# Performance work log

Hardware: AMD Instinct MI355X
Metric: run time of the kernel (lower is better)

## Reference

```python
import jax, jax.numpy as jnp
import numpy as np

N_NODES = 100000
N_EDGES = 1600000
DIM_NODE = 128
DIM_HID = 128
N_CLASSES = 10


def gcn_conv(x, src, dst, W, b, num_nodes):
    # PyG GCNConv: h = W x; out[i] = sum_j norm_ij * h[j] + b, with self-loops
    # and symmetric normalization norm_ij = deg(i)^-1/2 * deg(j)^-1/2.
    ones = jnp.ones(src.shape[0], dtype=x.dtype)
    deg = jax.ops.segment_sum(ones, dst, num_segments=num_nodes)  # in-degree incl self-loop
    dinv = jnp.where(deg > 0, jax.lax.rsqrt(deg), 0.0)
    norm = dinv[src] * dinv[dst]                                  # [E+N]
    h = x @ W                                                     # [N, out]
    msg = h[src] * norm[:, None]                                  # gather + scale
    out = jax.ops.segment_sum(msg, dst, num_segments=num_nodes)   # scatter-add
    return out + b


def setup_inputs() -> dict:
    key = jax.random.key(0)
    ks = jax.random.split(key, 8)
    x = jax.random.normal(ks[0], (N_NODES, DIM_NODE), dtype=jnp.float32)
    edge_index = jax.random.randint(ks[1], (2, N_EDGES), 0, N_NODES, dtype=jnp.int32)
    def lin(k, fan_in, fan_out):
        s = 1.0 / np.sqrt(fan_in)
        return jax.random.uniform(k, (fan_in, fan_out), jnp.float32, -s, s)
    W1 = lin(ks[2], DIM_NODE, DIM_HID)
    W2 = lin(ks[3], DIM_HID, DIM_HID)
    W3 = lin(ks[4], DIM_HID, DIM_HID)
    fW1 = lin(ks[5], DIM_HID, DIM_HID)
    fW2 = lin(ks[6], DIM_HID, N_CLASSES)
    z = lambda n: jnp.zeros((n,), jnp.float32)
    return {"x": x, "edge_index": edge_index,
            "W1": W1, "b1": z(DIM_HID), "W2": W2, "b2": z(DIM_HID),
            "W3": W3, "b3": z(DIM_HID), "fW1": fW1, "fb1": z(DIM_HID),
            "fW2": fW2, "fb2": z(N_CLASSES)}


def reference(x, edge_index, W1, b1, W2, b2, W3, b3, fW1, fb1, fW2, fb2):
    num_nodes = x.shape[0]
    loop = jnp.arange(num_nodes, dtype=edge_index.dtype)
    src = jnp.concatenate([edge_index[0], loop])  # add self-loops once
    dst = jnp.concatenate([edge_index[1], loop])
    h = jax.nn.relu(gcn_conv(x, src, dst, W1, b1, num_nodes))
    h = jax.nn.relu(gcn_conv(h, src, dst, W2, b2, num_nodes))
    h = jax.nn.relu(gcn_conv(h, src, dst, W3, b3, num_nodes))
    # FFN head (Dropout is identity in eval mode)
    h = jax.nn.relu(h @ fW1 + fb1)
    out = h @ fW2 + fb2
    return out
```

## Files before the change

kernel.cpp:

```cpp
#include <hip/hip_runtime.h>
#include <hip/hip_bf16.h>
#include <hip/hip_fp16.h>

#define DIM 128
#define ROWS 16
#define NCAP 64
#define NSH  6

typedef __attribute__((ext_vector_type(8))) short bf16x8;
typedef __attribute__((ext_vector_type(4))) float f32x4;
typedef _Float16 half_t;

union Frag { unsigned int u[4]; bf16x8 v; uint4 q; };
union H8   { uint4 q; half_t h[8]; };

__device__ __forceinline__ void cvt_hilo(const float* __restrict__ x, Frag& hi, Frag& lo) {
#pragma unroll
    for (int p = 0; p < 4; ++p) {
        float x0 = x[2 * p], x1 = x[2 * p + 1];
        unsigned int h0 = (__float_as_uint(x0) + 0x8000u) & 0xffff0000u;
        unsigned int h1 = (__float_as_uint(x1) + 0x8000u) & 0xffff0000u;
        hi.u[p] = (h0 >> 16) | h1;
        float d0 = x0 - __uint_as_float(h0);
        float d1 = x1 - __uint_as_float(h1);
        lo.u[p] = (__float_as_uint(d0) >> 16) | (__float_as_uint(d1) & 0xffff0000u);
    }
}

__global__ __launch_bounds__(256) void init_kernel(
    const float* __restrict__ W0, const float* __restrict__ W1,
    const float* __restrict__ W2, const float* __restrict__ W3,
    uint4* __restrict__ WFhi, uint4* __restrict__ WFlo,
    int* __restrict__ ncur, int N) {
    int t = blockIdx.x * 256 + threadIdx.x;
    if (t < 8192) {
        int wi = t >> 11;
        const float* W = (wi == 0) ? W0 : (wi == 1) ? W1 : (wi == 2) ? W2 : W3;
        int tt   = t & 2047;
        int lane = tt & 63;
        int f    = tt >> 6;
        int kc   = f >> 3;
        int wc   = (f >> 2) & 1;
        int ct   = f & 3;
        int m    = lane & 15;
        int quad = lane >> 4;
        int col  = wc * 64 + ct * 16 + m;
        int k0   = kc * 32 + quad * 8;
        float wv8[8];
#pragma unroll
        for (int j = 0; j < 8; ++j) wv8[j] = W[(size_t)(k0 + j) * DIM + col];
        Frag hi, lo;
        cvt_hilo(wv8, hi, lo);
        WFhi[t] = hi.q;
        WFlo[t] = lo.q;
    }
    int n = t - 8192;
    if (n >= 0 && n < N) ncur[n] = n << NSH;
}

__global__ __launch_bounds__(256) void dinv_kernel(
    const int* __restrict__ ncur, float* __restrict__ dinv, int N) {
    int n = blockIdx.x * 256 + threadIdx.x;
    if (n < N) {
        int deg = min(ncur[n] - (n << NSH), NCAP);
        dinv[n] = rsqrtf((float)(deg + 1));
    }
}

__global__ __launch_bounds__(256, 8) void mega_kernel(
    const float* __restrict__ X,
    const uint4* __restrict__ WFhi, const uint4* __restrict__ WFlo,
    half_t* __restrict__ Y,
    const int* __restrict__ src, const int* __restrict__ dst,
    int* __restrict__ ncur, int* __restrict__ colidx,
    int E, int N, int nGemm)
{
    __shared__ uint4 Sbuf[512];
    const int bid = blockIdx.x;
    const int tid = threadIdx.x;

    if ((bid % 5) == 4) {
        const int sIdx  = bid / 5;
        const int nScat = gridDim.x / 5;
        for (int e = sIdx * 256 + tid; e < E; e += nScat * 256) {
            int d = dst[e];
            int p = atomicAdd(&ncur[d], 1);
            if (p < (d << NSH) + NCAP) colidx[p] = src[e];
        }
        return;
    }
    const int g = bid - (bid + 1) / 5;
    if (g >= nGemm) return;
    const int row0 = g * ROWS;

    {
        const int row  = tid >> 4;
        const int oct  = tid & 15;
        const int node = row0 + row;
        float acc8[8];
        if (node < N) {
            const float* xp = X + (size_t)node * DIM + oct * 8;
            float4 a0 = *(const float4*)xp;
            float4 a1 = *(const float4*)(xp + 4);
            acc8[0] = a0.x; acc8[1] = a0.y; acc8[2] = a0.z; acc8[3] = a0.w;
            acc8[4] = a1.x; acc8[5] = a1.y; acc8[6] = a1.z; acc8[7] = a1.w;
        } else {
#pragma unroll
            for (int j = 0; j < 8; ++j) acc8[j] = 0.f;
        }
        Frag hi, lo;
        cvt_hilo(acc8, hi, lo);
        int fi = (oct >> 2) * 64 + (oct & 3) * 16 + (row ^ oct);
        Sbuf[fi]       = hi.q;
        Sbuf[256 + fi] = lo.q;
    }
    __syncthreads();

    const int lane = tid & 63;
    const int w    = tid >> 6;
    const int m    = lane & 15;
    const int quad = lane >> 4;
    f32x4 acc[2];
    acc[0] = f32x4{0.f, 0.f, 0.f, 0.f};
    acc[1] = f32x4{0.f, 0.f, 0.f, 0.f};
#pragma unroll
    for (int kc = 0; kc < 4; ++kc) {
        Frag ahi, alo;
        int fi = kc * 64 + quad * 16 + (m ^ (kc * 4 + quad));
        ahi.q = Sbuf[fi];
        alo.q = Sbuf[256 + fi];
#pragma unroll
        for (int j = 0; j < 2; ++j) {
            int ctg = w * 2 + j;
            Frag bhi, blo;
            int idx = (kc * 8 + ctg) * 64 + lane;
            bhi.q = WFhi[idx];
            blo.q = WFlo[idx];
            acc[j] = __builtin_amdgcn_mfma_f32_16x16x32_bf16(ahi.v, bhi.v, acc[j], 0, 0, 0);
            acc[j] = __builtin_amdgcn_mfma_f32_16x16x32_bf16(ahi.v, blo.v, acc[j], 0, 0, 0);
            acc[j] = __builtin_amdgcn_mfma_f32_16x16x32_bf16(alo.v, bhi.v, acc[j], 0, 0, 0);
        }
    }

#pragma unroll
    for (int r = 0; r < 4; ++r) {
        int grow = row0 + quad * 4 + r;
        if (grow >= N) continue;
#pragma unroll
        for (int j = 0; j < 2; ++j)
            Y[(size_t)grow * DIM + w * 32 + j * 16 + m] = (half_t)acc[j][r];
    }
}

template<bool SRCSCALE, bool FFN>
__global__ __launch_bounds__(256, 8) void fused16(
    const int* __restrict__ ncur, const int* __restrict__ colidx,
    const half_t* __restrict__ Hin, const float* __restrict__ bg,
    const float* __restrict__ dinv,
    const uint4* __restrict__ WFhi, const uint4* __restrict__ WFlo,
    const float* __restrict__ fb1,
    const float* __restrict__ fW2, const float* __restrict__ fb2,
    void* __restrict__ YV, int N)
{
    __shared__ uint4 Sbuf[512];
    __shared__ float Wl[FFN ? (DIM * 10 + 16) : 1];

    const int tid  = threadIdx.x;
    const int row0 = blockIdx.x * ROWS;

    if constexpr (FFN) {
        for (int i = tid; i < DIM * 10; i += 256) Wl[i] = fW2[i];
        if (tid < 10) Wl[DIM * 10 + tid] = fb2[tid];
    }

    {
        const int row  = tid >> 4;
        const int oct  = tid & 15;
        const int node = row0 + row;
        float acc8[8];
        if (node < N) {
            const half_t* hb = Hin + oct * 8;
            H8 sv; sv.q = *(const uint4*)(hb + (size_t)node * DIM);
            const float dvd = dinv[node];
            float a[8];
#pragma unroll
            for (int j = 0; j < 8; ++j)
                a[j] = SRCSCALE ? dvd * (float)sv.h[j] : (float)sv.h[j];
            const int beg = node << NSH;
            const int deg = min(ncur[node] - beg, NCAP);
            int e = 0;
            for (; e + 4 <= deg; e += 4) {
                int4 c = *(const int4*)&colidx[beg + e];
                H8 v0, v1, v2, v3;
                v0.q = *(const uint4*)(hb + (size_t)c.x * DIM);
                v1.q = *(const uint4*)(hb + (size_t)c.y * DIM);
                v2.q = *(const uint4*)(hb + (size_t)c.z * DIM);
                v3.q = *(const uint4*)(hb + (size_t)c.w * DIM);
                if constexpr (SRCSCALE) {
                    float d0 = dinv[c.x], d1 = dinv[c.y], d2 = dinv[c.z], d3 = dinv[c.w];
#pragma unroll
                    for (int j = 0; j < 8; ++j)
                        a[j] = fmaf(d3, (float)v3.h[j],
                               fmaf(d2, (float)v2.h[j],
                               fmaf(d1, (float)v1.h[j],
                               fmaf(d0, (float)v0.h[j], a[j]))));
                } else {
#pragma unroll
                    for (int j = 0; j < 8; ++j)
                        a[j] += ((float)v0.h[j] + (float)v1.h[j]) + ((float)v2.h[j] + (float)v3.h[j]);
                }
            }
            for (; e < deg; ++e) {
                int c = colidx[beg + e];
                H8 v0; v0.q = *(const uint4*)(hb + (size_t)c * DIM);
                if constexpr (SRCSCALE) {
                    float d0 = dinv[c];
#pragma unroll
                    for (int j = 0; j < 8; ++j) a[j] = fmaf(d0, (float)v0.h[j], a[j]);
                } else {
#pragma unroll
                    for (int j = 0; j < 8; ++j) a[j] += (float)v0.h[j];
                }
            }
            const float* bp = bg + oct * 8;
#pragma unroll
            for (int j = 0; j < 8; ++j)
                acc8[j] = fmaxf(fmaf(a[j], dvd, bp[j]), 0.f);
        } else {
#pragma unroll
            for (int j = 0; j < 8; ++j) acc8[j] = 0.f;
        }
        Frag hi, lo;
        cvt_hilo(acc8, hi, lo);
        int fi = (oct >> 2) * 64 + (oct & 3) * 16 + (row ^ oct);
        Sbuf[fi]       = hi.q;
        Sbuf[256 + fi] = lo.q;
    }
    __syncthreads();

    const int lane = tid & 63;
    const int w    = tid >> 6;
    const int m    = lane & 15;
    const int quad = lane >> 4;

    f32x4 acc[2];
    acc[0] = f32x4{0.f, 0.f, 0.f, 0.f};
    acc[1] = f32x4{0.f, 0.f, 0.f, 0.f};

#pragma unroll
    for (int kc = 0; kc < 4; ++kc) {
        Frag ahi, alo;
        int fi = kc * 64 + quad * 16 + (m ^ (kc * 4 + quad));
        ahi.q = Sbuf[fi];
        alo.q = Sbuf[256 + fi];
#pragma unroll
        for (int j = 0; j < 2; ++j) {
            int ctg = w * 2 + j;
            Frag bhi, blo;
            int idx = (kc * 8 + ctg) * 64 + lane;
            bhi.q = WFhi[idx];
            blo.q = WFlo[idx];
            acc[j] = __builtin_amdgcn_mfma_f32_16x16x32_bf16(ahi.v, bhi.v, acc[j], 0, 0, 0);
            acc[j] = __builtin_amdgcn_mfma_f32_16x16x32_bf16(ahi.v, blo.v, acc[j], 0, 0, 0);
            acc[j] = __builtin_amdgcn_mfma_f32_16x16x32_bf16(alo.v, bhi.v, acc[j], 0, 0, 0);
        }
    }

    if constexpr (!FFN) {
        half_t* Y = (half_t*)YV;
#pragma unroll
        for (int r = 0; r < 4; ++r) {
            int grow = row0 + quad * 4 + r;
            if (grow >= N) continue;
            float s = dinv[grow];
#pragma unroll
            for (int j = 0; j < 2; ++j)
                Y[(size_t)grow * DIM + w * 32 + j * 16 + m] = (half_t)(acc[j][r] * s);
        }
    } else {
        float* Y = (float*)YV;
        __syncthreads();
        float* hbuf = (float*)Sbuf;
#pragma unroll
        for (int r = 0; r < 4; ++r) {
            int lrow = quad * 4 + r;
#pragma unroll
            for (int j = 0; j < 2; ++j) {
                int col = w * 32 + j * 16 + m;
                hbuf[lrow * DIM + col] = fmaxf(acc[j][r] + fb1[col], 0.f);
            }
        }
        __syncthreads();
        if (tid < ROWS * 10) {
            int r  = tid / 10;
            int cc = tid - r * 10;
            int grow = row0 + r;
            if (grow < N) {
                float a = 0.f;
#pragma unroll 8
                for (int kk = 0; kk < DIM; ++kk) {
                    int k = (kk + r * 4) & 127;
                    a = fmaf(hbuf[r * DIM + k], Wl[k * 10 + cc], a);
                }
                Y[(size_t)grow * 10 + cc] = a + Wl[DIM * 10 + cc];
            }
        }
    }
}

extern "C" void kernel_launch(void* const* d_in, const int* in_sizes, int n_in,
                              void* d_out, int out_size, void* d_ws, size_t ws_size,
                              hipStream_t stream) {
    const float* x   = (const float*)d_in[0];
    const int*   ei  = (const int*)  d_in[1];
    const float* W1  = (const float*)d_in[2];
    const float* b1  = (const float*)d_in[3];
    const float* W2  = (const float*)d_in[4];
    const float* b2  = (const float*)d_in[5];
    const float* W3  = (const float*)d_in[6];
    const float* b3  = (const float*)d_in[7];
    const float* fW1 = (const float*)d_in[8];
    const float* fb1 = (const float*)d_in[9];
    const float* fW2 = (const float*)d_in[10];
    const float* fb2 = (const float*)d_in[11];
    float* out = (float*)d_out;

    const int N = in_sizes[0] / DIM;
    const int E = in_sizes[1] / 2;
    const int* srcI = ei;
    const int* dstI = ei + E;

    char* ws = (char*)d_ws;
    size_t off = 0;
    auto carve = [&](size_t bytes) { void* p = ws + off; off = (off + bytes + 255) & ~(size_t)255; return p; };
    int*   ncur       = (int*)  carve((size_t)N * 4);
    float* dinv       = (float*)carve((size_t)N * 4);
    int*   colidx     = (int*)  carve((size_t)N * NCAP * 4);
    uint4* wfhi       = (uint4*)carve((size_t)4 * 2048 * 16);
    uint4* wflo       = (uint4*)carve((size_t)4 * 2048 * 16);
    half_t* bufA      = (half_t*)carve((size_t)N * DIM * 2);
    half_t* bufB      = (half_t*)carve((size_t)N * DIM * 2);

    dim3 blk(256);
    int nGemm = (N + ROWS - 1) / ROWS;
    int gInit = (8192 + N + 255) / 256;
    int gN    = (N + 255) / 256;
    int gMega = (nGemm * 5 + 3) / 4;

    init_kernel<<<gInit, blk, 0, stream>>>(W1, W2, W3, fW1, wfhi, wflo, ncur, N);

    mega_kernel<<<gMega, blk, 0, stream>>>(x, wfhi + 0 * 2048, wflo + 0 * 2048, bufA,
                                           srcI, dstI, ncur, colidx, E, N, nGemm);

    dinv_kernel<<<gN, blk, 0, stream>>>(ncur, dinv, N);

    fused16<true, false><<<nGemm, blk, 0, stream>>>(ncur, colidx, bufA, b1, dinv,
                                                    wfhi + 1 * 2048, wflo + 1 * 2048,
                                                    nullptr, nullptr, nullptr, bufB, N);

    fused16<false, false><<<nGemm, blk, 0, stream>>>(ncur, colidx, bufB, b2, dinv,
                                                     wfhi + 2 * 2048, wflo + 2 * 2048,
                                                     nullptr, nullptr, nullptr, bufA, N);

    fused16<false, true><<<nGemm, blk, 0, stream>>>(ncur, colidx, bufA, b3, dinv,
                                                    wfhi + 3 * 2048, wflo + 3 * 2048,
                                                    fb1, fW2, fb2, out, N);
}
```

Before: 425.9 us.

## Partition edge scatter by destination slice per XCD with shared-memory staging ring

The scatter blocks now each own one of eight destination-node slices, picked from the block index, which appears meant to line up with the round-robin block-to-XCD placement. Each block scans the whole edge list for its group, keeps edges whose destination falls in its slice, and packs src and local dst into a shared ring buffer. It drains the ring in 256-entry batches to do the ncur atomics and colidx writes. The aim is to keep atomics and colidx writes for a node range local to one L2 instead of spread across all XCDs. In exchange, the dst array is read eight times, and there are extra barriers and shared-memory atomics per chunk.

Result: no change. 418.9 us (-1.7%).

```diff
diff --git a/kernel.cpp b/kernel.cpp
--- a/kernel.cpp
+++ b/kernel.cpp
@@ -80,12 +80,60 @@
     const int tid = threadIdx.x;
 
     if ((bid % 5) == 4) {
-        const int sIdx  = bid / 5;
+        __shared__ unsigned int ering[2048];
+        __shared__ int sh_head, sh_tail;
+        const int sid   = bid / 5;
         const int nScat = gridDim.x / 5;
-        for (int e = sIdx * 256 + tid; e < E; e += nScat * 256) {
-            int d = dst[e];
+        const int t8    = sid & 7;
+        const int jj    = sid >> 3;
+        const int nj    = (nScat >> 3) + (t8 < (nScat & 7) ? 1 : 0);
+        const int s     = bid & 7;
+        const int ssz   = (N + 7) >> 3;
+        const int lo    = s * ssz;
+        const int hi    = min(lo + ssz, N);
+        if (tid == 0) { sh_head = 0; sh_tail = 0; }
+        __syncthreads();
+        for (long long base = (long long)jj * 1024; base < E; base += (long long)nj * 1024) {
+            int e0 = (int)base + tid * 4;
+            if (e0 + 3 < E) {
+                int4 dd = *(const int4*)&dst[e0];
+#pragma unroll
+                for (int k = 0; k < 4; ++k) {
+                    int d = (&dd.x)[k];
+                    if (d >= lo && d < hi) {
+                        int p = atomicAdd(&sh_head, 1);
+                        ering[p & 2047] = (unsigned)src[e0 + k] | ((unsigned)(d - lo) << 17);
+                    }
+                }
+            } else {
+                for (int k = 0; k < 4; ++k) {
+                    int e = e0 + k;
+                    if (e < E) {
+                        int d = dst[e];
+                        if (d >= lo && d < hi) {
+                            int p = atomicAdd(&sh_head, 1);
+                            ering[p & 2047] = (unsigned)src[e] | ((unsigned)(d - lo) << 17);
+                        }
+                    }
+                }
+            }
+            __syncthreads();
+            while (sh_head - sh_tail >= 256) {
+                unsigned v = ering[(sh_tail + tid) & 2047];
+                int d = lo + (int)(v >> 17);
+                int p = atomicAdd(&ncur[d], 1);
+                if (p < (d << NSH) + NCAP) colidx[p] = (int)(v & 0x1FFFF);
+                __syncthreads();
+                if (tid == 0) sh_tail += 256;
+                __syncthreads();
+            }
+        }
+        int backlog = sh_head - sh_tail;
+        if (tid < backlog) {
+            unsigned v = ering[(sh_tail + tid) & 2047];
+            int d = lo + (int)(v >> 17);
             int p = atomicAdd(&ncur[d], 1);
-            if (p < (d << NSH) + NCAP) colidx[p] = src[e];
+            if (p < (d << NSH) + NCAP) colidx[p] = (int)(v & 0x1FFFF);
         }
         return;
     }
```
